# Kernel tuning notes

Hardware: AMD Instinct MI355X
Metric: run time of the kernel (lower is better)

## Reference

```python
import jax, jax.numpy as jnp
import numpy as np

DELTA = 1e-3  # kernel_delta

B, N, D, K = 256, 131072, 128, 50


def setup_inputs() -> dict:
    key = jax.random.key(0)
    k1, k2, k3 = jax.random.split(key, 3)
    return {
        "key": jax.random.normal(k1, (B, D), dtype=jnp.float32),
        "keys": jax.random.normal(k2, (N, D), dtype=jnp.float32),
        "values": jax.random.normal(k3, (N, 1), dtype=jnp.float32),
        "num_neighbours": K,
    }


def reference(key, keys, values, num_neighbours):
    # Squared L2 distance via GEMM expansion (same math as
    # torch.square(torch.norm(key[:,None]-keys, dim=-1)))
    q_sq = jnp.sum(key * key, axis=1, keepdims=True)          # [B,1]
    d_sq = jnp.sum(keys * keys, axis=1)                        # [N]
    cross = key @ keys.T                                       # [B,N] GEMM
    dist2 = jnp.maximum(q_sq + d_sq[None, :] - 2.0 * cross, 0.0)
    # inverse-distance-weighting kernel
    weights = 1.0 / (dist2 + DELTA)                            # [B,N]
    # top-k mask + renormalize (non-topk weights are zeroed, so the
    # normalized sum reduces to a sum over the top-k entries)
    top_w, top_idx = jax.lax.top_k(weights, num_neighbours)    # [B,K]
    w_norm = top_w / jnp.sum(top_w, axis=1, keepdims=True)     # [B,K]
    # gather matched values and weighted sum
    v = values[top_idx, 0]                                     # [B,K]
    output = jnp.sum(w_norm * v, axis=1, keepdims=True)        # [B,1]
    return output
```

## Files before the change

### kernel.cpp

```cpp
#include <hip/hip_runtime.h>

#define BQ 256
#define NK 131072
#define DIM 128
#define KT2 128
#define NCH2 (NK / KT2)
#define SAMP 8192
#define SBLK (SAMP / KT2)
#define CAPB 16
#define CAPL 8192
#define DELTA 1e-3f

typedef __attribute__((ext_vector_type(8))) short bf16x8;
typedef __attribute__((ext_vector_type(4))) float f32x4;

__device__ __forceinline__ unsigned short f2bf(float x) {
    unsigned u = __float_as_uint(x);
    u += 0x7fffu + ((u >> 16) & 1u);
    return (unsigned short)(u >> 16);
}
__device__ __forceinline__ float bf2f(unsigned short h) {
    return __uint_as_float(((unsigned)h) << 16);
}
__device__ __forceinline__ int kclamp(int K) {
    if (K < 1) K = 1;
    if (K > 256) K = 256;
    return K;
}

__global__ __launch_bounds__(256, 4)
void p0_prep(const float* __restrict__ qkey,
             unsigned short* __restrict__ qhG, unsigned short* __restrict__ qlG,
             float* __restrict__ qsqg)
{
    const int item = blockIdx.x * 256 + threadIdx.x;
    const int r = item >> 4, d0 = (item & 15) * 8;
    const float* src = qkey + (r << 7) + d0;
    float4 a = *(const float4*)src, b = *(const float4*)(src + 4);
    float x0 = a.x, x1 = a.y, x2 = a.z, x3 = a.w;
    float x4 = b.x, x5 = b.y, x6 = b.z, x7 = b.w;
    bf16x8 hv, lv;
    unsigned short h;
    h = f2bf(x0); hv[0] = (short)h; lv[0] = (short)f2bf(x0 - bf2f(h));
    h = f2bf(x1); hv[1] = (short)h; lv[1] = (short)f2bf(x1 - bf2f(h));
    h = f2bf(x2); hv[2] = (short)h; lv[2] = (short)f2bf(x2 - bf2f(h));
    h = f2bf(x3); hv[3] = (short)h; lv[3] = (short)f2bf(x3 - bf2f(h));
    h = f2bf(x4); hv[4] = (short)h; lv[4] = (short)f2bf(x4 - bf2f(h));
    h = f2bf(x5); hv[5] = (short)h; lv[5] = (short)f2bf(x5 - bf2f(h));
    h = f2bf(x6); hv[6] = (short)h; lv[6] = (short)f2bf(x6 - bf2f(h));
    h = f2bf(x7); hv[7] = (short)h; lv[7] = (short)f2bf(x7 - bf2f(h));
    *(bf16x8*)(qhG + (r << 7) + d0) = hv;
    *(bf16x8*)(qlG + (r << 7) + d0) = lv;
    float s = (x0*x0 + x1*x1) + (x2*x2 + x3*x3) + (x4*x4 + x5*x5) + (x6*x6 + x7*x7);
    #pragma unroll
    for (int off = 1; off < 16; off <<= 1) s += __shfl_xor(s, off, 16);
    if ((threadIdx.x & 15) == 0) qsqg[r] = s;
}

template<bool FILTER>
__global__ __launch_bounds__(512, 2)
void kmfma(const unsigned short* __restrict__ qhG, const unsigned short* __restrict__ qlG,
           const float* __restrict__ keys, const float* __restrict__ qsqg,
           const float* __restrict__ values, float* __restrict__ dout,
           const unsigned* __restrict__ tau, int* __restrict__ cntmat,
           uint2* __restrict__ cand)
{
    __shared__ __align__(16) unsigned short khs[KT2 * DIM];
    __shared__ __align__(16) unsigned short kls[KT2 * DIM];
    __shared__ float    ksq_s[KT2];
    __shared__ float    qsq_s[BQ];
    __shared__ unsigned tau_s[BQ];
    __shared__ int      lcnt[BQ];

    const int tid   = threadIdx.x;
    const int kbase = blockIdx.x * KT2;

    if (tid < BQ) {
        qsq_s[tid] = qsqg[tid];
        if (FILTER) { tau_s[tid] = tau[tid]; lcnt[tid] = 0; }
    }

    #pragma unroll
    for (int p = 0; p < 4; ++p) {
        int flat = p * 4096 + tid * 8;
        int rr = flat >> 7;
        int d0 = flat & 127;
        const float* src = keys + (((size_t)(kbase + rr)) << 7) + d0;
        float4 a = *(const float4*)src, b = *(const float4*)(src + 4);
        float x0 = a.x, x1 = a.y, x2 = a.z, x3 = a.w;
        float x4 = b.x, x5 = b.y, x6 = b.z, x7 = b.w;
        bf16x8 hv, lv;
        unsigned short h;
        h = f2bf(x0); hv[0] = (short)h; lv[0] = (short)f2bf(x0 - bf2f(h));
        h = f2bf(x1); hv[1] = (short)h; lv[1] = (short)f2bf(x1 - bf2f(h));
        h = f2bf(x2); hv[2] = (short)h; lv[2] = (short)f2bf(x2 - bf2f(h));
        h = f2bf(x3); hv[3] = (short)h; lv[3] = (short)f2bf(x3 - bf2f(h));
        h = f2bf(x4); hv[4] = (short)h; lv[4] = (short)f2bf(x4 - bf2f(h));
        h = f2bf(x5); hv[5] = (short)h; lv[5] = (short)f2bf(x5 - bf2f(h));
        h = f2bf(x6); hv[6] = (short)h; lv[6] = (short)f2bf(x6 - bf2f(h));
        h = f2bf(x7); hv[7] = (short)h; lv[7] = (short)f2bf(x7 - bf2f(h));
        float sq = (x0*x0 + x1*x1) + (x2*x2 + x3*x3) + (x4*x4 + x5*x5) + (x6*x6 + x7*x7);
        unsigned byte = (unsigned)((rr << 8) + (d0 << 1));
        byte ^= (unsigned)((rr & 7) << 4);
        *(bf16x8*)((char*)khs + byte) = hv;
        *(bf16x8*)((char*)kls + byte) = lv;
        #pragma unroll
        for (int off = 1; off < 16; off <<= 1) sq += __shfl_xor(sq, off, 16);
        if ((tid & 15) == 0) ksq_s[rr] = sq;
    }

    const int lane = tid & 63, wv = tid >> 6;
    const int qb0 = wv * 32;
    const int fr = lane & 15, fg = lane >> 4;
    bf16x8 qh[2][4], ql[2][4];
    #pragma unroll
    for (int qf = 0; qf < 2; ++qf)
        #pragma unroll
        for (int s = 0; s < 4; ++s) {
            int off = ((qb0 + qf * 16 + fr) << 7) + s * 32 + fg * 8;
            qh[qf][s] = *(const bf16x8*)(qhG + off);
            ql[qf][s] = *(const bf16x8*)(qlG + off);
        }

    f32x4 acc[2][8];
    #pragma unroll
    for (int qf = 0; qf < 2; ++qf)
        #pragma unroll
        for (int kf = 0; kf < 8; ++kf) acc[qf][kf] = f32x4{0.f, 0.f, 0.f, 0.f};

    __syncthreads();

    #pragma unroll
    for (int s = 0; s < 4; ++s) {
        #pragma unroll
        for (int kf = 0; kf < 8; ++kf) {
            const int krow = kf * 16 + fr;
            const int d0   = s * 32 + fg * 8;
            unsigned byte = ((unsigned)((krow << 8) + (d0 << 1))) ^ (unsigned)((krow & 7) << 4);
            bf16x8 bh = *(bf16x8*)((char*)khs + byte);
            bf16x8 bl = *(bf16x8*)((char*)kls + byte);
            #pragma unroll
            for (int qf = 0; qf < 2; ++qf) {
                acc[qf][kf] = __builtin_amdgcn_mfma_f32_16x16x32_bf16(qh[qf][s], bh, acc[qf][kf], 0, 0, 0);
                acc[qf][kf] = __builtin_amdgcn_mfma_f32_16x16x32_bf16(ql[qf][s], bh, acc[qf][kf], 0, 0, 0);
                acc[qf][kf] = __builtin_amdgcn_mfma_f32_16x16x32_bf16(qh[qf][s], bl, acc[qf][kf], 0, 0, 0);
            }
        }
    }

    #pragma unroll
    for (int qf = 0; qf < 2; ++qf) {
        #pragma unroll
        for (int kf = 0; kf < 8; ++kf) {
            const int kcol = kf * 16 + fr;
            const int k = kbase + kcol;
            const float kq = ksq_s[kcol];
            f32x4 a = acc[qf][kf];
            #pragma unroll
            for (int rg = 0; rg < 4; ++rg) {
                const int q = qb0 + qf * 16 + fg * 4 + rg;
                float dv = fmaxf(qsq_s[q] + kq - 2.f * a[rg], 0.f);
                if (FILTER) {
                    if (dv <= __uint_as_float(tau_s[q])) {
                        int slot = atomicAdd(&lcnt[q], 1);
                        if (slot < CAPB)
                            cand[((size_t)q * NCH2 + blockIdx.x) * CAPB + slot] =
                                make_uint2(__float_as_uint(dv), __float_as_uint(values[k]));
                    }
                } else {
                    dout[(size_t)q * SAMP + k] = dv;
                }
            }
        }
    }
    if (FILTER) {
        __syncthreads();
        if (tid < BQ) {
            int c = lcnt[tid]; if (c > CAPB) c = CAPB;
            cntmat[(size_t)tid * NCH2 + blockIdx.x] = c;
        }
    }
}

__global__ __launch_bounds__(256, 4)
void k2_tau(const float* __restrict__ dsamp, const int* __restrict__ pK,
            unsigned* __restrict__ tau)
{
    const int q = blockIdx.x, tid = threadIdx.x;
    const int lane = tid & 63, wid = tid >> 6;
    const int K = kclamp(*pK);

    unsigned eb[32];
    const float4* row4 = (const float4*)(dsamp + (size_t)q * SAMP);
    #pragma unroll
    for (int i = 0; i < 8; ++i) {
        float4 v = row4[tid + 256 * i];
        eb[4*i+0] = __float_as_uint(v.x); eb[4*i+1] = __float_as_uint(v.y);
        eb[4*i+2] = __float_as_uint(v.z); eb[4*i+3] = __float_as_uint(v.w);
    }

    __shared__ int red[4];
    __shared__ unsigned go;
    unsigned lo = 0u, hi = 0x7f7fffffu;
    while (lo < hi) {
        unsigned mid = lo + ((hi - lo) >> 1);
        int c = 0;
        #pragma unroll
        for (int i = 0; i < 32; ++i) c += (eb[i] <= mid) ? 1 : 0;
        #pragma unroll
        for (int off = 32; off; off >>= 1) c += __shfl_down(c, off, 64);
        if (lane == 0) red[wid] = c;
        __syncthreads();
        if (tid == 0) go = ((red[0] + red[1] + red[2] + red[3]) >= K) ? 1u : 0u;
        __syncthreads();
        if (go) hi = mid; else lo = mid + 1;
        __syncthreads();
    }
    if (tid == 0) tau[q] = lo;
}

__global__ __launch_bounds__(256, 2)
void k4_final(const uint2* __restrict__ cand, const int* __restrict__ cntmat,
              const unsigned* __restrict__ tau, const int* __restrict__ pK,
              float* __restrict__ out)
{
    const int q = blockIdx.x, tid = threadIdx.x;
    const int lane = tid & 63, wid = tid >> 6;
    const int K = kclamp(*pK);

    __shared__ uint2 list[CAPL];
    __shared__ int   wtot[4];
    __shared__ int   red[4];
    __shared__ unsigned go;

    int4 c4 = ((const int4*)(cntmat + (size_t)q * NCH2))[tid];
    int mysum = c4.x + c4.y + c4.z + c4.w;

    int incl = mysum;
    #pragma unroll
    for (int off = 1; off < 64; off <<= 1) {
        int t = __shfl_up(incl, off, 64);
        if (lane >= off) incl += t;
    }
    if (lane == 63) wtot[wid] = incl;
    __syncthreads();
    int base = incl - mysum;
    #pragma unroll
    for (int w = 0; w < 4; ++w) if (w < wid) base += wtot[w];
    const int total = wtot[0] + wtot[1] + wtot[2] + wtot[3];

    {
        int off = base;
        const uint2* seg = cand + ((size_t)q * NCH2 + tid * 4) * CAPB;
        int cc[4] = { c4.x, c4.y, c4.z, c4.w };
        #pragma unroll
        for (int s2 = 0; s2 < 4; ++s2) {
            #pragma unroll 1
            for (int j = 0; j < cc[s2]; ++j) {
                if (off < CAPL) list[off] = seg[s2 * CAPB + j];
                ++off;
            }
        }
    }
    __syncthreads();
    int n = total; if (n > CAPL) n = CAPL;

    unsigned lo = 0u, hi = tau[q];
    while (lo < hi) {
        unsigned mid = lo + ((hi - lo) >> 1);
        int c = 0;
        for (int i = tid; i < n; i += 256) c += (list[i].x <= mid) ? 1 : 0;
        #pragma unroll
        for (int off = 32; off; off >>= 1) c += __shfl_down(c, off, 64);
        if (lane == 0) red[wid] = c;
        __syncthreads();
        if (tid == 0) go = ((red[0] + red[1] + red[2] + red[3]) >= K) ? 1u : 0u;
        __syncthreads();
        if (go) hi = mid; else lo = mid + 1;
        __syncthreads();
    }
    const unsigned T = lo;

    double sw = 0.0, swv = 0.0, sevt = 0.0;
    int cl = 0, ce = 0;
    for (int i = tid; i < n; i += 256) {
        unsigned b = list[i].x;
        float d = __uint_as_float(b), v = __uint_as_float(list[i].y);
        if (b < T) {
            double w = 1.0 / ((double)d + (double)DELTA);
            cl += 1; sw += w; swv += w * (double)v;
        } else if (b == T) { ce += 1; sevt += (double)v; }
    }
    #pragma unroll
    for (int off = 32; off; off >>= 1) {
        sw   += __shfl_down(sw,   off, 64);
        swv  += __shfl_down(swv,  off, 64);
        sevt += __shfl_down(sevt, off, 64);
        cl   += __shfl_down(cl,   off, 64);
        ce   += __shfl_down(ce,   off, 64);
    }
    __shared__ double dred[3][4];
    __shared__ int    ired[2][4];
    if (lane == 0) { dred[0][wid] = sw; dred[1][wid] = swv; dred[2][wid] = sevt;
                     ired[0][wid] = cl; ired[1][wid] = ce; }
    __syncthreads();
    if (tid == 0) {
        double SW = 0, SWV = 0, SEVT = 0; int CL = 0, CE = 0;
        #pragma unroll
        for (int w = 0; w < 4; ++w) { SW += dred[0][w]; SWV += dred[1][w]; SEVT += dred[2][w];
                                      CL += ired[0][w]; CE += ired[1][w]; }
        double wT = 1.0 / ((double)__uint_as_float(T) + (double)DELTA);
        double need = (double)(K - CL);
        double num = SWV + wT * (need / (double)CE) * SEVT;
        double den = SW + wT * need;
        out[q] = (float)(num / den);
    }
}

extern "C" void kernel_launch(void* const* d_in, const int* in_sizes, int n_in,
                              void* d_out, int out_size, void* d_ws, size_t ws_size,
                              hipStream_t stream)
{
    const float* qkey   = (const float*)d_in[0];
    const float* keys   = (const float*)d_in[1];
    const float* values = (const float*)d_in[2];
    const int*   pK     = (const int*)d_in[3];
    float* out = (float*)d_out;

    char* w = (char*)d_ws;
    float*          qsqg  = (float*)w;
    unsigned short* qhG   = (unsigned short*)(w + 4096);
    unsigned short* qlG   = (unsigned short*)(w + 4096 + 65536);
    float*          dsamp = (float*)(w + 4096 + 131072);
    unsigned*       tau   = (unsigned*)(w + 4096 + 131072 + 8388608);
    int*            cntmat= (int*)(w + 4096 + 131072 + 8388608 + 4096);
    uint2*          cand  = (uint2*)(w + 4096 + 131072 + 8388608 + 4096 + 1048576);

    p0_prep<<<dim3(16), dim3(256), 0, stream>>>(qkey, qhG, qlG, qsqg);
    kmfma<false><<<dim3(SBLK), dim3(512), 0, stream>>>(qhG, qlG, keys, qsqg, values,
                                                       dsamp, tau, cntmat, cand);
    k2_tau<<<dim3(BQ), dim3(256), 0, stream>>>(dsamp, pK, tau);
    kmfma<true><<<dim3(NCH2), dim3(512), 0, stream>>>(qhG, qlG, keys, qsqg, values,
                                                      dsamp, tau, cntmat, cand);
    k4_final<<<dim3(BQ), dim3(256), 0, stream>>>(cand, cntmat, tau, pK, out);
}
```

Baseline: 129.1 us.

## Make MFMA blocks persistent over key chunks with prefetch; histogram-select threshold in final

The distance kernel now uses 1024-thread blocks, each wave owning 16 queries, and each block loops over several key chunks. The next chunk's fp32 keys are prefetched into registers while the current chunk's MFMAs run, and per-chunk candidate counters are double-buffered. The final kernel replaces the per-query binary search over the candidate list with a 4096-bin histogram that finds the k-th bucket, followed by an exact rank selection inside that bucket. It falls back to binary search when that bucket holds more than 256 entries. The aim is to cut launch/prologue overhead and serial bisection passes, at the cost of fewer blocks, more registers, and larger shared memory.

After: 127.8 us. Within noise of the previous version (-1.0%).

```diff
diff --git a/kernel.cpp b/kernel.cpp
--- a/kernel.cpp
+++ b/kernel.cpp
@@ -7,8 +7,11 @@
 #define NCH2 (NK / KT2)
 #define SAMP 8192
 #define SBLK (SAMP / KT2)
+#define CPB_MAIN 4
+#define GRID_MAIN (NCH2 / CPB_MAIN)
 #define CAPB 16
 #define CAPL 8192
+#define NB2 4096
 #define DELTA 1e-3f
 
 typedef __attribute__((ext_vector_type(8))) short bf16x8;
@@ -26,6 +29,18 @@
     if (K < 1) K = 1;
     if (K > 256) K = 256;
     return K;
+}
+__device__ __forceinline__ void cvt8(const float4 a, const float4 b,
+                                     bf16x8& hv, bf16x8& lv, float& sq) {
+    float xs[8] = { a.x, a.y, a.z, a.w, b.x, b.y, b.z, b.w };
+    sq = 0.f;
+    #pragma unroll
+    for (int i = 0; i < 8; ++i) {
+        unsigned short h = f2bf(xs[i]);
+        hv[i] = (short)h;
+        lv[i] = (short)f2bf(xs[i] - bf2f(h));
+        sq = fmaf(xs[i], xs[i], sq);
+    }
 }
 
 __global__ __launch_bounds__(256, 4)
@@ -37,134 +52,122 @@
     const int r = item >> 4, d0 = (item & 15) * 8;
     const float* src = qkey + (r << 7) + d0;
     float4 a = *(const float4*)src, b = *(const float4*)(src + 4);
-    float x0 = a.x, x1 = a.y, x2 = a.z, x3 = a.w;
-    float x4 = b.x, x5 = b.y, x6 = b.z, x7 = b.w;
-    bf16x8 hv, lv;
-    unsigned short h;
-    h = f2bf(x0); hv[0] = (short)h; lv[0] = (short)f2bf(x0 - bf2f(h));
-    h = f2bf(x1); hv[1] = (short)h; lv[1] = (short)f2bf(x1 - bf2f(h));
-    h = f2bf(x2); hv[2] = (short)h; lv[2] = (short)f2bf(x2 - bf2f(h));
-    h = f2bf(x3); hv[3] = (short)h; lv[3] = (short)f2bf(x3 - bf2f(h));
-    h = f2bf(x4); hv[4] = (short)h; lv[4] = (short)f2bf(x4 - bf2f(h));
-    h = f2bf(x5); hv[5] = (short)h; lv[5] = (short)f2bf(x5 - bf2f(h));
-    h = f2bf(x6); hv[6] = (short)h; lv[6] = (short)f2bf(x6 - bf2f(h));
-    h = f2bf(x7); hv[7] = (short)h; lv[7] = (short)f2bf(x7 - bf2f(h));
+    bf16x8 hv, lv; float s;
+    cvt8(a, b, hv, lv, s);
     *(bf16x8*)(qhG + (r << 7) + d0) = hv;
     *(bf16x8*)(qlG + (r << 7) + d0) = lv;
-    float s = (x0*x0 + x1*x1) + (x2*x2 + x3*x3) + (x4*x4 + x5*x5) + (x6*x6 + x7*x7);
     #pragma unroll
     for (int off = 1; off < 16; off <<= 1) s += __shfl_xor(s, off, 16);
     if ((threadIdx.x & 15) == 0) qsqg[r] = s;
 }
 
 template<bool FILTER>
-__global__ __launch_bounds__(512, 2)
+__global__ __launch_bounds__(1024)
 void kmfma(const unsigned short* __restrict__ qhG, const unsigned short* __restrict__ qlG,
            const float* __restrict__ keys, const float* __restrict__ qsqg,
            const float* __restrict__ values, float* __restrict__ dout,
            const unsigned* __restrict__ tau, int* __restrict__ cntmat,
-           uint2* __restrict__ cand)
+           uint2* __restrict__ cand, int cpb)
 {
     __shared__ __align__(16) unsigned short khs[KT2 * DIM];
     __shared__ __align__(16) unsigned short kls[KT2 * DIM];
     __shared__ float    ksq_s[KT2];
     __shared__ float    qsq_s[BQ];
     __shared__ unsigned tau_s[BQ];
-    __shared__ int      lcnt[BQ];
-
-    const int tid   = threadIdx.x;
-    const int kbase = blockIdx.x * KT2;
+    __shared__ int      lcnt[2][BQ];
+
+    const int tid  = threadIdx.x;
+    const int lane = tid & 63, wv = tid >> 6;
+    const int fr = lane & 15, fg = lane >> 4;
 
     if (tid < BQ) {
         qsq_s[tid] = qsqg[tid];
-        if (FILTER) { tau_s[tid] = tau[tid]; lcnt[tid] = 0; }
-    }
-
-    #pragma unroll
-    for (int p = 0; p < 4; ++p) {
-        int flat = p * 4096 + tid * 8;
-        int rr = flat >> 7;
-        int d0 = flat & 127;
-        const float* src = keys + (((size_t)(kbase + rr)) << 7) + d0;
-        float4 a = *(const float4*)src, b = *(const float4*)(src + 4);
-        float x0 = a.x, x1 = a.y, x2 = a.z, x3 = a.w;
-        float x4 = b.x, x5 = b.y, x6 = b.z, x7 = b.w;
-        bf16x8 hv, lv;
-        unsigned short h;
-        h = f2bf(x0); hv[0] = (short)h; lv[0] = (short)f2bf(x0 - bf2f(h));
-        h = f2bf(x1); hv[1] = (short)h; lv[1] = (short)f2bf(x1 - bf2f(h));
-        h = f2bf(x2); hv[2] = (short)h; lv[2] = (short)f2bf(x2 - bf2f(h));
-        h = f2bf(x3); hv[3] = (short)h; lv[3] = (short)f2bf(x3 - bf2f(h));
-        h = f2bf(x4); hv[4] = (short)h; lv[4] = (short)f2bf(x4 - bf2f(h));
-        h = f2bf(x5); hv[5] = (short)h; lv[5] = (short)f2bf(x5 - bf2f(h));
-        h = f2bf(x6); hv[6] = (short)h; lv[6] = (short)f2bf(x6 - bf2f(h));
-        h = f2bf(x7); hv[7] = (short)h; lv[7] = (short)f2bf(x7 - bf2f(h));
-        float sq = (x0*x0 + x1*x1) + (x2*x2 + x3*x3) + (x4*x4 + x5*x5) + (x6*x6 + x7*x7);
-        unsigned byte = (unsigned)((rr << 8) + (d0 << 1));
-        byte ^= (unsigned)((rr & 7) << 4);
-        *(bf16x8*)((char*)khs + byte) = hv;
-        *(bf16x8*)((char*)kls + byte) = lv;
-        #pragma unroll
-        for (int off = 1; off < 16; off <<= 1) sq += __shfl_xor(sq, off, 16);
-        if ((tid & 15) == 0) ksq_s[rr] = sq;
-    }
-
-    const int lane = tid & 63, wv = tid >> 6;
-    const int qb0 = wv * 32;
-    const int fr = lane & 15, fg = lane >> 4;
-    bf16x8 qh[2][4], ql[2][4];
-    #pragma unroll
-    for (int qf = 0; qf < 2; ++qf)
+        if (FILTER) { tau_s[tid] = tau[tid]; lcnt[0][tid] = 0; lcnt[1][tid] = 0; }
+    }
+
+    bf16x8 qh[4], ql[4];
+    #pragma unroll
+    for (int s = 0; s < 4; ++s) {
+        int off = ((wv * 16 + fr) << 7) + s * 32 + fg * 8;
+        qh[s] = *(const bf16x8*)(qhG + off);
+        ql[s] = *(const bf16x8*)(qlG + off);
+    }
+
+    const int r0 = tid >> 4;
+    const int d0 = (tid & 15) * 8;
+
+    float4 ra0, rb0, ra1, rb1;
+    int ch = blockIdx.x * cpb;
+    {
+        const float* s0 = keys + (size_t)ch * (KT2 * DIM) + tid * 8;
+        ra0 = *(const float4*)s0;          rb0 = *(const float4*)(s0 + 4);
+        ra1 = *(const float4*)(s0 + 8192); rb1 = *(const float4*)(s0 + 8192 + 4);
+    }
+
+    for (int c = 0; c < cpb; ++c, ++ch) {
+        {
+            bf16x8 hv, lv; float sq;
+            cvt8(ra0, rb0, hv, lv, sq);
+            unsigned byte = ((unsigned)((r0 << 8) + (d0 << 1))) ^ (unsigned)((r0 & 7) << 4);
+            *(bf16x8*)((char*)khs + byte) = hv;
+            *(bf16x8*)((char*)kls + byte) = lv;
+            #pragma unroll
+            for (int off = 1; off < 16; off <<= 1) sq += __shfl_xor(sq, off, 16);
+            if ((tid & 15) == 0) ksq_s[r0] = sq;
+            const int r1 = r0 + 64;
+            cvt8(ra1, rb1, hv, lv, sq);
+            byte = ((unsigned)((r1 << 8) + (d0 << 1))) ^ (unsigned)((r1 & 7) << 4);
+            *(bf16x8*)((char*)khs + byte) = hv;
+            *(bf16x8*)((char*)kls + byte) = lv;
+            #pragma unroll
+            for (int off = 1; off < 16; off <<= 1) sq += __shfl_xor(sq, off, 16);
+            if ((tid & 15) == 0) ksq_s[r1] = sq;
+        }
+        __syncthreads();
+
+        if (c + 1 < cpb) {
+            const float* s0 = keys + (size_t)(ch + 1) * (KT2 * DIM) + tid * 8;
+            ra0 = *(const float4*)s0;          rb0 = *(const float4*)(s0 + 4);
+            ra1 = *(const float4*)(s0 + 8192); rb1 = *(const float4*)(s0 + 8192 + 4);
+        }
+
+        f32x4 acc[8];
+        #pragma unroll
+        for (int kf = 0; kf < 8; ++kf) acc[kf] = f32x4{0.f, 0.f, 0.f, 0.f};
+
         #pragma unroll
         for (int s = 0; s < 4; ++s) {
-            int off = ((qb0 + qf * 16 + fr) << 7) + s * 32 + fg * 8;
-            qh[qf][s] = *(const bf16x8*)(qhG + off);
-            ql[qf][s] = *(const bf16x8*)(qlG + off);
-        }
-
-    f32x4 acc[2][8];
-    #pragma unroll
-    for (int qf = 0; qf < 2; ++qf)
-        #pragma unroll
-        for (int kf = 0; kf < 8; ++kf) acc[qf][kf] = f32x4{0.f, 0.f, 0.f, 0.f};
-
-    __syncthreads();
-
-    #pragma unroll
-    for (int s = 0; s < 4; ++s) {
-        #pragma unroll
-        for (int kf = 0; kf < 8; ++kf) {
-            const int krow = kf * 16 + fr;
-            const int d0   = s * 32 + fg * 8;
-            unsigned byte = ((unsigned)((krow << 8) + (d0 << 1))) ^ (unsigned)((krow & 7) << 4);
-            bf16x8 bh = *(bf16x8*)((char*)khs + byte);
-            bf16x8 bl = *(bf16x8*)((char*)kls + byte);
             #pragma unroll
-            for (int qf = 0; qf < 2; ++qf) {
-                acc[qf][kf] = __builtin_amdgcn_mfma_f32_16x16x32_bf16(qh[qf][s], bh, acc[qf][kf], 0, 0, 0);
-                acc[qf][kf] = __builtin_amdgcn_mfma_f32_16x16x32_bf16(ql[qf][s], bh, acc[qf][kf], 0, 0, 0);
-                acc[qf][kf] = __builtin_amdgcn_mfma_f32_16x16x32_bf16(qh[qf][s], bl, acc[qf][kf], 0, 0, 0);
+            for (int kf = 0; kf < 8; ++kf) {
+                const int krow = kf * 16 + fr;
+                const int dd   = s * 32 + fg * 8;
+                unsigned byte = ((unsigned)((krow << 8) + (dd << 1))) ^ (unsigned)((krow & 7) << 4);
+                bf16x8 bh = *(bf16x8*)((char*)khs + byte);
+                bf16x8 bl = *(bf16x8*)((char*)kls + byte);
+                acc[kf] = __builtin_amdgcn_mfma_f32_16x16x32_bf16(qh[s], bh, acc[kf], 0, 0, 0);
+                acc[kf] = __builtin_amdgcn_mfma_f32_16x16x32_bf16(ql[s], bh, acc[kf], 0, 0, 0);
+                acc[kf] = __builtin_amdgcn_mfma_f32_16x16x32_bf16(qh[s], bl, acc[kf], 0, 0, 0);
             }
         }
-    }
-
-    #pragma unroll
-    for (int qf = 0; qf < 2; ++qf) {
+
+        float qsqv[4];
+        #pragma unroll
+        for (int rg = 0; rg < 4; ++rg) qsqv[rg] = qsq_s[wv * 16 + fg * 4 + rg];
         #pragma unroll
         for (int kf = 0; kf < 8; ++kf) {
             const int kcol = kf * 16 + fr;
-            const int k = kbase + kcol;
+            const int k = ch * KT2 + kcol;
             const float kq = ksq_s[kcol];
-            f32x4 a = acc[qf][kf];
+            f32x4 a = acc[kf];
             #pragma unroll
             for (int rg = 0; rg < 4; ++rg) {
-                const int q = qb0 + qf * 16 + fg * 4 + rg;
-                float dv = fmaxf(qsq_s[q] + kq - 2.f * a[rg], 0.f);
+                const int q = wv * 16 + fg * 4 + rg;
+                float dv = fmaxf(qsqv[rg] + kq - 2.f * a[rg], 0.f);
                 if (FILTER) {
                     if (dv <= __uint_as_float(tau_s[q])) {
-                        int slot = atomicAdd(&lcnt[q], 1);
+                        int slot = atomicAdd(&lcnt[c & 1][q], 1);
                         if (slot < CAPB)
-                            cand[((size_t)q * NCH2 + blockIdx.x) * CAPB + slot] =
+                            cand[((size_t)q * NCH2 + ch) * CAPB + slot] =
                                 make_uint2(__float_as_uint(dv), __float_as_uint(values[k]));
                     }
                 } else {
@@ -172,12 +175,11 @@
                 }
             }
         }
-    }
-    if (FILTER) {
         __syncthreads();
-        if (tid < BQ) {
-            int c = lcnt[tid]; if (c > CAPB) c = CAPB;
-            cntmat[(size_t)tid * NCH2 + blockIdx.x] = c;
+        if (FILTER && tid < BQ) {
+            int cc2 = lcnt[c & 1][tid]; if (cc2 > CAPB) cc2 = CAPB;
+            lcnt[c & 1][tid] = 0;
+            cntmat[(size_t)tid * NCH2 + ch] = cc2;
         }
     }
 }
@@ -219,7 +221,7 @@
     if (tid == 0) tau[q] = lo;
 }
 
-__global__ __launch_bounds__(256, 2)
+__global__ __launch_bounds__(256)
 void k4_final(const uint2* __restrict__ cand, const int* __restrict__ cntmat,
               const unsigned* __restrict__ tau, const int* __restrict__ pK,
               float* __restrict__ out)
@@ -228,14 +230,18 @@
     const int lane = tid & 63, wid = tid >> 6;
     const int K = kclamp(*pK);
 
-    __shared__ uint2 list[CAPL];
-    __shared__ int   wtot[4];
-    __shared__ int   red[4];
+    __shared__ uint2    list[CAPL];
+    __shared__ int      hist2[NB2];
+    __shared__ unsigned bcand[256];
+    __shared__ int      wtot[4];
+    __shared__ int      red[4];
     __shared__ unsigned go;
+    __shared__ int      s_bb, s_cb, s_m;
+    __shared__ unsigned s_T;
+    __shared__ unsigned long long s_S;
 
     int4 c4 = ((const int4*)(cntmat + (size_t)q * NCH2))[tid];
     int mysum = c4.x + c4.y + c4.z + c4.w;
-
     int incl = mysum;
     #pragma unroll
     for (int off = 1; off < 64; off <<= 1) {
@@ -243,6 +249,11 @@
         if (lane >= off) incl += t;
     }
     if (lane == 63) wtot[wid] = incl;
+    for (int i = tid; i < NB2; i += 256) hist2[i] = 0;
+    if (tid == 0) {
+        s_m = 0; s_bb = NB2; s_cb = 0;
+        s_S = (((unsigned long long)NB2) << 32) / ((unsigned long long)tau[q] + 1ULL);
+    }
     __syncthreads();
     int base = incl - mysum;
     #pragma unroll
@@ -263,23 +274,76 @@
         }
     }
     __syncthreads();
-    int n = total; if (n > CAPL) n = CAPL;
-
-    unsigned lo = 0u, hi = tau[q];
-    while (lo < hi) {
-        unsigned mid = lo + ((hi - lo) >> 1);
-        int c = 0;
-        for (int i = tid; i < n; i += 256) c += (list[i].x <= mid) ? 1 : 0;
-        #pragma unroll
-        for (int off = 32; off; off >>= 1) c += __shfl_down(c, off, 64);
-        if (lane == 0) red[wid] = c;
-        __syncthreads();
-        if (tid == 0) go = ((red[0] + red[1] + red[2] + red[3]) >= K) ? 1u : 0u;
-        __syncthreads();
-        if (go) hi = mid; else lo = mid + 1;
-        __syncthreads();
-    }
-    const unsigned T = lo;
+    const int n = (total > CAPL) ? CAPL : total;
+    const unsigned long long S = s_S;
+
+    for (int i = tid; i < n; i += 256)
+        atomicAdd(&hist2[(unsigned)(((unsigned long long)list[i].x * S) >> 32)], 1);
+    __syncthreads();
+
+    int h[16], sum16 = 0;
+    #pragma unroll
+    for (int b = 0; b < 16; ++b) { h[b] = hist2[tid * 16 + b]; sum16 += h[b]; }
+    int incl2 = sum16;
+    #pragma unroll
+    for (int off = 1; off < 64; off <<= 1) {
+        int t = __shfl_up(incl2, off, 64);
+        if (lane >= off) incl2 += t;
+    }
+    if (lane == 63) red[wid] = incl2;
+    __syncthreads();
+    int base2 = incl2 - sum16;
+    #pragma unroll
+    for (int w = 0; w < 4; ++w) if (w < wid) base2 += red[w];
+    if (base2 < K) {
+        int c = base2;
+        #pragma unroll
+        for (int b = 0; b < 16; ++b) {
+            if (c < K && c + h[b] >= K) { s_bb = tid * 16 + b; s_cb = c; }
+            c += h[b];
+        }
+    }
+    __syncthreads();
+    const int bb = s_bb, cbelow = s_cb, R2 = K - cbelow;
+
+    for (int i = tid; i < n; i += 256) {
+        unsigned bits = list[i].x;
+        if ((int)(unsigned)(((unsigned long long)bits * S) >> 32) == bb) {
+            int sl = atomicAdd(&s_m, 1);
+            if (sl < 256) bcand[sl] = bits;
+        }
+    }
+    __syncthreads();
+    const int m = s_m;
+    if (m <= 256) {
+        if (tid < m) {
+            unsigned bi = bcand[tid];
+            int cl = 0, ceq = 0;
+            for (int j = 0; j < m; ++j) {
+                unsigned bj = bcand[j];
+                cl += (bj < bi) ? 1 : 0; ceq += (bj == bi) ? 1 : 0;
+            }
+            if (cl < R2 && R2 <= cl + ceq) s_T = bi;
+        }
+    } else {
+        unsigned lo = 0u, hi = tau[q];
+        while (lo < hi) {
+            unsigned mid = lo + ((hi - lo) >> 1);
+            int c = 0;
+            for (int i = tid; i < n; i += 256) c += (list[i].x <= mid) ? 1 : 0;
+            #pragma unroll
+            for (int off = 32; off; off >>= 1) c += __shfl_down(c, off, 64);
+            if (lane == 0) red[wid] = c;
+            __syncthreads();
+            if (tid == 0) go = ((red[0] + red[1] + red[2] + red[3]) >= K) ? 1u : 0u;
+            __syncthreads();
+            if (go) hi = mid; else lo = mid + 1;
+            __syncthreads();
+        }
+        if (tid == 0) s_T = lo;
+    }
+    __syncthreads();
+    const unsigned T = s_T;
 
     double sw = 0.0, swv = 0.0, sevt = 0.0;
     int cl = 0, ce = 0;
@@ -331,16 +395,16 @@
     float*          qsqg  = (float*)w;
     unsigned short* qhG   = (unsigned short*)(w + 4096);
     unsigned short* qlG   = (unsigned short*)(w + 4096 + 65536);
-    float*          dsamp = (float*)(w + 4096 + 131072);
-    unsigned*       tau   = (unsigned*)(w + 4096 + 131072 + 8388608);
-    int*            cntmat= (int*)(w + 4096 + 131072 + 8388608 + 4096);
-    uint2*          cand  = (uint2*)(w + 4096 + 131072 + 8388608 + 4096 + 1048576);
+    float*          dsamp = (float*)(w + 135168);
+    unsigned*       tauB  = (unsigned*)(w + 8523776);
+    int*            cntmat= (int*)(w + 8527872);
+    uint2*          cand  = (uint2*)(w + 9576448);
 
     p0_prep<<<dim3(16), dim3(256), 0, stream>>>(qkey, qhG, qlG, qsqg);
-    kmfma<false><<<dim3(SBLK), dim3(512), 0, stream>>>(qhG, qlG, keys, qsqg, values,
-                                                       dsamp, tau, cntmat, cand);
-    k2_tau<<<dim3(BQ), dim3(256), 0, stream>>>(dsamp, pK, tau);
-    kmfma<true><<<dim3(NCH2), dim3(512), 0, stream>>>(qhG, qlG, keys, qsqg, values,
-                                                      dsamp, tau, cntmat, cand);
-    k4_final<<<dim3(BQ), dim3(256), 0, stream>>>(cand, cntmat, tau, pK, out);
-}
+    kmfma<false><<<dim3(SBLK), dim3(1024), 0, stream>>>(qhG, qlG, keys, qsqg, values,
+                                                        dsamp, tauB, cntmat, cand, 1);
+    k2_tau<<<dim3(BQ), dim3(256), 0, stream>>>(dsamp, pK, tauB);
+    kmfma<true><<<dim3(GRID_MAIN), dim3(1024), 0, stream>>>(qhG, qlG, keys, qsqg, values,
+                                                            dsamp, tauB, cntmat, cand, CPB_MAIN);
+    k4_final<<<dim3(BQ), dim3(256), 0, stream>>>(cand, cntmat, tauB, pK, out);
+}
```
